# Kernel tuning notes

Measured on AMD Instinct MI355X. Metric: run time of the kernel, lower is better.

The kernel has to match this reference:

```python
import jax, jax.numpy as jnp
import numpy as np

D_MODEL = 1024
NUM_HEADS = 16
D_K = D_MODEL // NUM_HEADS


def setup_inputs() -> dict:
    key = jax.random.key(0)
    ks = jax.random.split(key, 11)
    B, S = 2, 2048
    scale = 1.0 / np.sqrt(D_MODEL)
    inp = {
        "q": jax.random.normal(ks[0], (B, S, D_MODEL), jnp.float32),
        "k": jax.random.normal(ks[1], (B, S, D_MODEL), jnp.float32),
        "v": jax.random.normal(ks[2], (B, S, D_MODEL), jnp.float32),
        "W_q": jax.random.normal(ks[3], (D_MODEL, D_MODEL), jnp.float32) * scale,
        "b_q": jnp.zeros((D_MODEL,), jnp.float32),
        "W_k": jax.random.normal(ks[4], (D_MODEL, D_MODEL), jnp.float32) * scale,
        "b_k": jnp.zeros((D_MODEL,), jnp.float32),
        "W_v": jax.random.normal(ks[5], (D_MODEL, D_MODEL), jnp.float32) * scale,
        "b_v": jnp.zeros((D_MODEL,), jnp.float32),
        "W_o": jax.random.normal(ks[6], (D_MODEL, D_MODEL), jnp.float32) * scale,
        "b_o": jnp.zeros((D_MODEL,), jnp.float32),
    }
    return inp


def _split_heads(x):
    B, S, _ = x.shape
    return x.reshape(B, S, NUM_HEADS, D_K).transpose(0, 2, 1, 3)  # [B,H,S,Dk]


def reference(q, k, v, W_q, b_q, W_k, b_k, W_v, b_v, W_o, b_o):
    # Linear projections (torch Linear: x @ W.T + b; here W stored as [in,out])
    qh = _split_heads(q @ W_q + b_q)  # [B,H,S,Dk]
    kh = _split_heads(k @ W_k + b_k)
    vh = _split_heads(v @ W_v + b_v)

    scores = jnp.einsum("bhqd,bhkd->bhqk", qh, kh) / jnp.sqrt(
        jnp.asarray(D_K, qh.dtype)
    )  # [B,H,S,S]
    probs = jax.nn.softmax(scores, axis=-1)
    ctx = jnp.einsum("bhqk,bhkd->bhqd", probs, vh)  # [B,H,S,Dk]

    B, H, S, Dk = ctx.shape
    out = ctx.transpose(0, 2, 1, 3).reshape(B, S, D_MODEL)
    return out @ W_o + b_o
```

## Files before the change

### kernel.cpp

```cpp
#include <hip/hip_runtime.h>
#include <stdint.h>

#define DM   1024
#define TOK  4096
#define SEQ  2048
#define NH   16
#define DKH  64
#define WELEM ((size_t)DM * DM)

typedef __bf16 bf16_t;
typedef bf16_t bf16x8 __attribute__((ext_vector_type(8)));
typedef _Float16 f16x8 __attribute__((ext_vector_type(8)));
typedef float  f32x16 __attribute__((ext_vector_type(16)));
typedef uint32_t u32x4 __attribute__((ext_vector_type(4)));

__device__ __forceinline__ uint16_t f2bf(float x) {
  uint32_t u = __builtin_bit_cast(uint32_t, x);
  u += 0x7fffu + ((u >> 16) & 1u);
  return (uint16_t)(u >> 16);
}
__device__ __forceinline__ uint16_t f2h(float x) {
  _Float16 h = (_Float16)x;
  return __builtin_bit_cast(uint16_t, h);
}
__device__ __forceinline__ uint32_t pkrtz(float a, float b) {
  auto h = __builtin_amdgcn_cvt_pkrtz(a, b);
  return __builtin_bit_cast(uint32_t, h);
}
__device__ __forceinline__ bf16x8 ldfrag(const uint16_t* p) {
  uint4 v = *(const uint4*)p;
  return __builtin_bit_cast(bf16x8, v);
}
__device__ __forceinline__ f16x8 ldfragh(const uint16_t* p) {
  uint4 v = *(const uint4*)p;
  return __builtin_bit_cast(f16x8, v);
}
__device__ __forceinline__ uint32_t cvtpk(float lo, float hi) {
  uint32_t r;
  asm("v_cvt_pk_bf16_f32 %0, %1, %2" : "=v"(r) : "v"(lo), "v"(hi));
  return r;
}
__device__ __forceinline__ void plswap(uint32_t& a, uint32_t& b) {
  asm("v_permlane32_swap_b32 %0, %1" : "+v"(a), "+v"(b));
}
__device__ __forceinline__ void gload_lds16(const void* g, void* l) {
  __builtin_amdgcn_global_load_lds(
      (const __attribute__((address_space(1))) uint32_t*)(g),
      (__attribute__((address_space(3))) uint32_t*)(l), 16, 0, 0);
}

__global__ void wsplit_kernel(const float* __restrict__ W0, const float* __restrict__ W1,
                              const float* __restrict__ W2, const float* __restrict__ W3,
                              uint16_t* __restrict__ hi) {
  const float* W = (blockIdx.z == 0) ? W0 : (blockIdx.z == 1) ? W1 : (blockIdx.z == 2) ? W2 : W3;
  uint16_t* hp = hi + blockIdx.z * WELEM;
  __shared__ float t[32][33];
  int n0 = blockIdx.x * 32, k0 = blockIdx.y * 32;
  int tx = threadIdx.x, ty = threadIdx.y;
#pragma unroll
  for (int i = 0; i < 4; i++) {
    int r = ty + i * 8;
    t[r][tx] = W[(size_t)(k0 + r) * DM + n0 + tx];
  }
  __syncthreads();
#pragma unroll
  for (int i = 0; i < 4; i++) {
    int r = ty + i * 8;
    hp[(size_t)(n0 + r) * DM + k0 + tx] = f2h(t[tx][r]);
  }
}

__global__ __launch_bounds__(256, 3) void proj_kernel(
    const float* __restrict__ A0, const float* __restrict__ A1, const float* __restrict__ A2,
    const uint16_t* __restrict__ Whi,
    const float* __restrict__ bA, const float* __restrict__ bB, const float* __restrict__ bC,
    uint16_t* __restrict__ oq, uint16_t* __restrict__ ok, uint16_t* __restrict__ ovt) {
  __shared__ __align__(16) char smem[49152];
  char* lA = smem;
  uint16_t* lBh = (uint16_t*)(smem + 32768);

  const int tid = threadIdx.x, lane = tid & 63, wid = tid >> 6;
  const int l31 = lane & 31, hi = lane >> 5;
  const int wr = wid >> 1, wc = wid & 1;
  const int bid = blockIdx.x, xcd = bid & 7, idx = bid >> 3;
  const int tm = xcd * 4 + (idx & 3), tn = idx >> 2;

  const int z = (int)blockIdx.y;
  const float* Ap = (z == 0) ? A0 : (z == 1) ? A1 : A2;
  const uint16_t* Bh = Whi + (size_t)z * WELEM;
  const float* bias = (z == 1) ? bB : (z == 2) ? bC : bA;

  f32x16 acc[2][2];
#pragma unroll
  for (int i = 0; i < 2; i++)
#pragma unroll
    for (int j = 0; j < 2; j++)
#pragma unroll
      for (int e = 0; e < 16; e++) acc[i][j][e] = 0.f;

  auto stage = [&](int buf, int kt) {
#pragma unroll
    for (int p = 0; p < 4; p++) {
      int sid = p * 256 + tid;
      int r = sid >> 3, cs = sid & 7;
      int g = cs ^ (r & 7);
      const float* src = Ap + (size_t)(tm * 128 + r) * DM + kt * 32 + g * 4;
      gload_lds16(src, lA + buf * 16384 + (p * 256 + wid * 64) * 16);
    }
#pragma unroll
    for (int p = 0; p < 2; p++) {
      int sid = p * 256 + tid;
      int r = sid >> 2, cs = sid & 3;
      int cg = cs ^ ((r >> 1) & 3);
      size_t offB = (size_t)(tn * 128 + r) * DM + kt * 32 + cg * 8;
      gload_lds16(Bh + offB, (char*)lBh + buf * 8192 + (p * 256 + wid * 64) * 16);
    }
  };

  stage(0, 0);
  for (int kt = 0; kt < DM / 32; kt++) {
    const int cur = kt & 1;
    __syncthreads();
    if (kt + 1 < DM / 32) stage(cur ^ 1, kt + 1);

    f16x8 af[2][2], bh[2][2];
#pragma unroll
    for (int ks = 0; ks < 2; ks++) {
      int cg4 = ks * 2 + hi;
#pragma unroll
      for (int rt = 0; rt < 2; rt++) {
        int rA = wr * 64 + rt * 32 + l31;
        const char* rowp = lA + cur * 16384 + rA * 128;
        uint4 u0 = *(const uint4*)(rowp + (((cg4 * 2)     ^ (rA & 7)) * 16));
        uint4 u1 = *(const uint4*)(rowp + (((cg4 * 2 + 1) ^ (rA & 7)) * 16));
        float4 f0 = __builtin_bit_cast(float4, u0);
        float4 f1 = __builtin_bit_cast(float4, u1);
        u32x4 uu;
        uu[0] = pkrtz(f0.x, f0.y); uu[1] = pkrtz(f0.z, f0.w);
        uu[2] = pkrtz(f1.x, f1.y); uu[3] = pkrtz(f1.z, f1.w);
        af[rt][ks] = __builtin_bit_cast(f16x8, uu);
      }
#pragma unroll
      for (int ct = 0; ct < 2; ct++) {
        int rB = wc * 64 + ct * 32 + l31;
        int cg = ks * 2 + hi;
        bh[ct][ks] = ldfragh(lBh + cur * 4096 + rB * 32 + (cg ^ ((rB >> 1) & 3)) * 8);
      }
    }
#pragma unroll
    for (int ks = 0; ks < 2; ks++)
#pragma unroll
      for (int rt = 0; rt < 2; rt++)
#pragma unroll
        for (int ct = 0; ct < 2; ct++)
          acc[rt][ct] = __builtin_amdgcn_mfma_f32_32x32x16_f16(af[rt][ks], bh[ct][ks], acc[rt][ct], 0, 0, 0);
  }

  if (z == 2) {
    __syncthreads();
    uint16_t* t16 = (uint16_t*)smem;
#pragma unroll
    for (int ct = 0; ct < 2; ct++) {
      int nl = wc * 64 + ct * 32 + l31;
      float bv = bias[tn * 128 + nl];
#pragma unroll
      for (int rt = 0; rt < 2; rt++)
#pragma unroll
        for (int g = 0; g < 16; g++) {
          int ml = wr * 64 + rt * 32 + (g & 3) + 8 * (g >> 2) + 4 * hi;
          t16[nl * 136 + ml] = f2bf(acc[rt][ct][g] + bv);
        }
    }
    __syncthreads();
    int nl2 = tid >> 1, mh = tid & 1;
    int ng = tn * 128 + nl2;
    int hh = ng >> 6, d = ng & 63;
    int b_ = tm >> 4, s0 = (tm & 15) * 128 + mh * 64;
    uint16_t* dst = ovt + (size_t)((b_ * NH + hh) * DKH + d) * SEQ + s0;
    const uint16_t* src = &t16[nl2 * 136 + mh * 64];
#pragma unroll
    for (int j = 0; j < 8; j++)
      ((uint4*)dst)[j] = ((const uint4*)src)[j];
  } else {
#pragma unroll
    for (int ct = 0; ct < 2; ct++) {
      int n = tn * 128 + wc * 64 + ct * 32 + l31;
      float bv = bias[n];
#pragma unroll
      for (int rt = 0; rt < 2; rt++)
#pragma unroll
        for (int g = 0; g < 16; g++) {
          int m = tm * 128 + wr * 64 + rt * 32 + (g & 3) + 8 * (g >> 2) + 4 * hi;
          float val = acc[rt][ct][g] + bv;
          if (z == 0) oq[(size_t)m * DM + n] = f2bf(val * 0.125f);
          else        ok[(size_t)m * DM + n] = f2bf(val);
        }
    }
  }
}

__global__ __launch_bounds__(256, 4) void proj_o_kernel(
    const uint16_t* __restrict__ A, const uint16_t* __restrict__ Bh,
    const float* __restrict__ bias, float* __restrict__ out) {
  __shared__ __attribute__((aligned(16))) uint16_t lA[2][128 * 32];
  __shared__ __attribute__((aligned(16))) uint16_t lBh[2][64 * 32];

  const int tid = threadIdx.x, lane = tid & 63, wid = tid >> 6;
  const int l31 = lane & 31, hi = lane >> 5;
  const int wr = wid >> 1, wc = wid & 1;
  const int bid = blockIdx.x, xcd = bid & 7, idx = bid >> 3;
  const int tm = xcd * 4 + (idx & 3), tn = idx >> 2;

  f32x16 acc[2];
#pragma unroll
  for (int i = 0; i < 2; i++)
#pragma unroll
    for (int e = 0; e < 16; e++) acc[i][e] = 0.f;

  auto stage = [&](int buf, int kt) {
#pragma unroll
    for (int p = 0; p < 2; p++) {
      int sid = p * 256 + tid;
      int r = sid >> 2, cs = sid & 3;
      int cg = cs ^ ((r >> 1) & 3);
      size_t offA = (size_t)(tm * 128 + r) * DM + kt * 32 + cg * 8;
      gload_lds16(A + offA, &lA[buf][(p * 256 + wid * 64) * 8]);
    }
    {
      int r = tid >> 2, cs = tid & 3;
      int cg = cs ^ ((r >> 1) & 3);
      size_t offB = (size_t)(tn * 64 + r) * DM + kt * 32 + cg * 8;
      gload_lds16(Bh + offB, &lBh[buf][wid * 64 * 8]);
    }
  };

  stage(0, 0);
  for (int kt = 0; kt < DM / 32; kt++) {
    const int cur = kt & 1;
    __syncthreads();
    if (kt + 1 < DM / 32) stage(cur ^ 1, kt + 1);

    f16x8 af[2][2], bh[2];
#pragma unroll
    for (int ks = 0; ks < 2; ks++) {
      int cg = ks * 2 + hi;
#pragma unroll
      for (int rt = 0; rt < 2; rt++) {
        int rA = wr * 64 + rt * 32 + l31;
        af[rt][ks] = ldfragh(&lA[cur][rA * 32 + (cg ^ ((rA >> 1) & 3)) * 8]);
      }
      int rB = wc * 32 + l31;
      bh[ks] = ldfragh(&lBh[cur][rB * 32 + (cg ^ ((rB >> 1) & 3)) * 8]);
    }
#pragma unroll
    for (int ks = 0; ks < 2; ks++)
#pragma unroll
      for (int rt = 0; rt < 2; rt++)
        acc[rt] = __builtin_amdgcn_mfma_f32_32x32x16_f16(af[rt][ks], bh[ks], acc[rt], 0, 0, 0);
  }

  const int n = tn * 64 + wc * 32 + l31;
  const float bv = bias[n];
#pragma unroll
  for (int rt = 0; rt < 2; rt++)
#pragma unroll
    for (int g = 0; g < 16; g++) {
      int m = tm * 128 + wr * 64 + rt * 32 + (g & 3) + 8 * (g >> 2) + 4 * hi;
      out[(size_t)m * DM + n] = acc[rt][g] + bv;
    }
}

__global__ __launch_bounds__(256, 2) void attn_kernel(
    const uint16_t* __restrict__ Qp, const uint16_t* __restrict__ Kp,
    const uint16_t* __restrict__ Vt, uint16_t* __restrict__ ctx) {
  __shared__ __align__(16) char smem[65536];
  uint16_t* lK = (uint16_t*)smem;
  uint16_t* lV = (uint16_t*)(smem + 32768);
  const int tid = threadIdx.x, lane = tid & 63, w = tid >> 6;
  const int q31 = lane & 31, hi = lane >> 5;
  const int bid = blockIdx.x, xcd = bid & 7, idx = bid >> 3;
  const int bh_ = xcd * 4 + (idx >> 4), qt = idx & 15;
  const int b = bh_ >> 4, h = bh_ & 15;
  const int bh = bh_;
  const float L2E = 1.44269504089f;
  const float MS = 20.0f * 1.44269504089f;

  auto stage = [&](int buf, int kt) {
#pragma unroll
    for (int p = 0; p < 4; p++) {
      int sid = p * 256 + tid;
      {
        int r = sid >> 3, cs = sid & 7;
        size_t gk = (size_t)(b * SEQ + kt * 128 + r) * DM + h * DKH + (cs ^ (r & 7)) * 8;
        gload_lds16(Kp + gk, lK + buf * 8192 + (p * 256 + w * 64) * 8);
      }
      {
        int r = sid >> 4, cs = sid & 15;
        size_t gv = (size_t)(bh * DKH + r) * SEQ + kt * 128 + (cs ^ (r & 7)) * 8;
        gload_lds16(Vt + gv, lV + buf * 8192 + (p * 256 + w * 64) * 8);
      }
    }
  };

  stage(0, 0);
  bf16x8 qf[4];
  const int qrow = b * SEQ + qt * 128 + w * 32 + q31;
#pragma unroll
  for (int d4 = 0; d4 < 4; d4++)
    qf[d4] = ldfrag(Qp + (size_t)qrow * DM + h * DKH + d4 * 16 + hi * 8);

  f32x16 zz;
#pragma unroll
  for (int i = 0; i < 16; i++) zz[i] = 0.f;
  f32x16 o0 = zz, o1 = zz;
  float l = 0.f;

  for (int kt = 0; kt < SEQ / 128; kt++) {
    const int cur = kt & 1;
    __syncthreads();
    if (kt + 1 < SEQ / 128) stage(cur ^ 1, kt + 1);

    __builtin_amdgcn_s_setprio(1);
    float s0 = 0.f, s1 = 0.f, s2 = 0.f, s3 = 0.f;
#pragma unroll
    for (int kb = 0; kb < 4; kb++) {
      f32x16 a = zz;
#pragma unroll
      for (int d4 = 0; d4 < 4; d4++) {
        int r = kb * 32 + q31;
        int slot = (d4 * 2 + hi) ^ (r & 7);
        bf16x8 kf = ldfrag(lK + cur * 8192 + r * 64 + slot * 8);
        a = __builtin_amdgcn_mfma_f32_32x32x16_bf16(kf, qf[d4], a, 0, 0, 0);
      }
#pragma unroll
      for (int r = 0; r < 16; r += 4) {
        float p0 = __builtin_amdgcn_exp2f(a[r + 0] * L2E - MS);
        float p1 = __builtin_amdgcn_exp2f(a[r + 1] * L2E - MS);
        float p2 = __builtin_amdgcn_exp2f(a[r + 2] * L2E - MS);
        float p3 = __builtin_amdgcn_exp2f(a[r + 3] * L2E - MS);
        a[r + 0] = p0; a[r + 1] = p1;
        a[r + 2] = p2; a[r + 3] = p3;
        s0 += p0; s1 += p1; s2 += p2; s3 += p3;
      }
      uint32_t wv[8];
#pragma unroll
      for (int i = 0; i < 8; i++) wv[i] = cvtpk(a[2 * i], a[2 * i + 1]);
      plswap(wv[0], wv[2]);
      plswap(wv[1], wv[3]);
      plswap(wv[4], wv[6]);
      plswap(wv[5], wv[7]);
      u32x4 c0, c1;
      c0[0] = wv[0]; c0[1] = wv[1]; c0[2] = wv[2]; c0[3] = wv[3];
      c1[0] = wv[4]; c1[1] = wv[5]; c1[2] = wv[6]; c1[3] = wv[7];
      bf16x8 p0f = __builtin_bit_cast(bf16x8, c0);
      bf16x8 p1f = __builtin_bit_cast(bf16x8, c1);
#pragma unroll
      for (int ks = 0; ks < 2; ks++) {
        bf16x8 pa = ks ? p1f : p0f;
        int cg = (kb * 2 + ks) * 2 + hi;
        {
          int r = q31;
          bf16x8 vf = ldfrag(lV + cur * 8192 + r * 128 + (cg ^ (r & 7)) * 8);
          o0 = __builtin_amdgcn_mfma_f32_32x32x16_bf16(vf, pa, o0, 0, 0, 0);
        }
        {
          int r = 32 + q31;
          bf16x8 vf = ldfrag(lV + cur * 8192 + r * 128 + (cg ^ (r & 7)) * 8);
          o1 = __builtin_amdgcn_mfma_f32_32x32x16_bf16(vf, pa, o1, 0, 0, 0);
        }
      }
    }
    __builtin_amdgcn_s_setprio(0);
    l += (s0 + s1) + (s2 + s3);
  }

  l += __shfl_xor(l, 32, 64);
  float rl = 1.f / l;
  __syncthreads();
  uint16_t* th = (uint16_t*)smem;
  int ql = w * 32 + q31;
#pragma unroll
  for (int g4 = 0; g4 < 4; g4++) {
    int d0 = g4 * 8 + hi * 4;
    ushort4 h0, h1;
#pragma unroll
    for (int e = 0; e < 4; e++) {
      ((uint16_t*)&h0)[e] = f2h(o0[g4 * 4 + e] * rl);
      ((uint16_t*)&h1)[e] = f2h(o1[g4 * 4 + e] * rl);
    }
    *(ushort4*)&th[ql * 72 + d0] = h0;
    *(ushort4*)&th[ql * 72 + 32 + d0] = h1;
  }
  __syncthreads();
  int qr = tid >> 1, dh = tid & 1;
  size_t obase = (size_t)(b * SEQ + qt * 128 + qr) * DM + h * DKH + dh * 32;
  const uint16_t* sh = &th[qr * 72 + dh * 32];
#pragma unroll
  for (int j = 0; j < 4; j++)
    ((uint4*)(ctx + obase))[j] = ((const uint4*)sh)[j];
}

extern "C" void kernel_launch(void* const* d_in, const int* in_sizes, int n_in,
                              void* d_out, int out_size, void* d_ws, size_t ws_size,
                              hipStream_t stream) {
  (void)in_sizes; (void)n_in; (void)out_size; (void)ws_size;
  const float* q  = (const float*)d_in[0];
  const float* k  = (const float*)d_in[1];
  const float* v  = (const float*)d_in[2];
  const float* Wq = (const float*)d_in[3];
  const float* bq = (const float*)d_in[4];
  const float* Wk = (const float*)d_in[5];
  const float* bk = (const float*)d_in[6];
  const float* Wv = (const float*)d_in[7];
  const float* bv = (const float*)d_in[8];
  const float* Wo = (const float*)d_in[9];
  const float* bo = (const float*)d_in[10];

  char* ws = (char*)d_ws;
  uint16_t* wt  = (uint16_t*)(ws + ((size_t)0 << 20));
  uint16_t* qp  = (uint16_t*)(ws + ((size_t)8 << 20));
  uint16_t* kp  = (uint16_t*)(ws + ((size_t)16 << 20));
  uint16_t* vt  = (uint16_t*)(ws + ((size_t)24 << 20));
  uint16_t* ctx = (uint16_t*)(ws + ((size_t)32 << 20));

  wsplit_kernel<<<dim3(32, 32, 4), dim3(32, 8), 0, stream>>>(Wq, Wk, Wv, Wo, wt);
  proj_kernel<<<dim3(256, 3), 256, 0, stream>>>(q, k, v, wt,
                                                bq, bk, bv, qp, kp, vt);
  attn_kernel<<<512, 256, 0, stream>>>(qp, kp, vt, ctx);
  proj_o_kernel<<<512, 256, 0, stream>>>(ctx, wt + 3 * WELEM, bo, (float*)d_out);
}
```

Measured before the change: 123.6 us.

## Convert A tile to fp16 in registers before LDS store in projection GEMM

The fp32 activation tile is no longer copied straight into LDS. It is now loaded into registers, converted to fp16 once per element, and stored to LDS in the same swizzled fp16 layout as the weights, with the store overlapping the MFMA work of the current stage. This halves the LDS footprint of the A buffer, so occupancy can rise from 3 to 4 blocks, and removes the repeated fp32-to-fp16 conversion on every fragment read. In exchange it adds register pressure for the prefetched float4s and issues synchronous global loads instead of direct-to-LDS loads.

```diff
diff --git a/kernel.cpp b/kernel.cpp
--- a/kernel.cpp
+++ b/kernel.cpp
@@ -70,14 +70,14 @@
   }
 }
 
-__global__ __launch_bounds__(256, 3) void proj_kernel(
+__global__ __launch_bounds__(256, 4) void proj_kernel(
     const float* __restrict__ A0, const float* __restrict__ A1, const float* __restrict__ A2,
     const uint16_t* __restrict__ Whi,
     const float* __restrict__ bA, const float* __restrict__ bB, const float* __restrict__ bC,
     uint16_t* __restrict__ oq, uint16_t* __restrict__ ok, uint16_t* __restrict__ ovt) {
-  __shared__ __align__(16) char smem[49152];
-  char* lA = smem;
-  uint16_t* lBh = (uint16_t*)(smem + 32768);
+  __shared__ __align__(16) char smem[36864];
+  uint16_t* lA  = (uint16_t*)smem;
+  uint16_t* lBh = (uint16_t*)(smem + 16384);
 
   const int tid = threadIdx.x, lane = tid & 63, wid = tid >> 6;
   const int l31 = lane & 31, hi = lane >> 5;
@@ -98,53 +98,68 @@
 #pragma unroll
       for (int e = 0; e < 16; e++) acc[i][j][e] = 0.f;
 
-  auto stage = [&](int buf, int kt) {
-#pragma unroll
-    for (int p = 0; p < 4; p++) {
+  float4 ar[2][2];
+
+  auto regloadA = [&](int kt) {
+#pragma unroll
+    for (int p = 0; p < 2; p++) {
       int sid = p * 256 + tid;
-      int r = sid >> 3, cs = sid & 7;
-      int g = cs ^ (r & 7);
-      const float* src = Ap + (size_t)(tm * 128 + r) * DM + kt * 32 + g * 4;
-      gload_lds16(src, lA + buf * 16384 + (p * 256 + wid * 64) * 16);
-    }
+      int r = sid >> 2, cs = sid & 3;
+      const float* src = Ap + (size_t)(tm * 128 + r) * DM + kt * 32 + cs * 8;
+      ar[p][0] = *(const float4*)(src);
+      ar[p][1] = *(const float4*)(src + 4);
+    }
+  };
+  auto writeA = [&](int buf) {
+#pragma unroll
+    for (int p = 0; p < 2; p++) {
+      int sid = p * 256 + tid;
+      int r = sid >> 2, cs = sid & 3;
+      int slot = cs ^ ((r >> 1) & 3);
+      u32x4 uu;
+      uu[0] = pkrtz(ar[p][0].x, ar[p][0].y);
+      uu[1] = pkrtz(ar[p][0].z, ar[p][0].w);
+      uu[2] = pkrtz(ar[p][1].x, ar[p][1].y);
+      uu[3] = pkrtz(ar[p][1].z, ar[p][1].w);
+      *(u32x4*)&lA[buf * 4096 + r * 32 + slot * 8] = uu;
+    }
+  };
+  auto stageB = [&](int buf, int kt) {
 #pragma unroll
     for (int p = 0; p < 2; p++) {
       int sid = p * 256 + tid;
       int r = sid >> 2, cs = sid & 3;
       int cg = cs ^ ((r >> 1) & 3);
       size_t offB = (size_t)(tn * 128 + r) * DM + kt * 32 + cg * 8;
-      gload_lds16(Bh + offB, (char*)lBh + buf * 8192 + (p * 256 + wid * 64) * 16);
+      gload_lds16(Bh + offB, &lBh[buf * 4096 + (p * 256 + wid * 64) * 8]);
     }
   };
 
-  stage(0, 0);
+  regloadA(0);
+  stageB(0, 0);
+  writeA(0);
+
   for (int kt = 0; kt < DM / 32; kt++) {
     const int cur = kt & 1;
     __syncthreads();
-    if (kt + 1 < DM / 32) stage(cur ^ 1, kt + 1);
+    if (kt + 1 < DM / 32) {
+      regloadA(kt + 1);
+      stageB(cur ^ 1, kt + 1);
+    }
 
     f16x8 af[2][2], bh[2][2];
 #pragma unroll
     for (int ks = 0; ks < 2; ks++) {
-      int cg4 = ks * 2 + hi;
+      int cg = ks * 2 + hi;
 #pragma unroll
       for (int rt = 0; rt < 2; rt++) {
         int rA = wr * 64 + rt * 32 + l31;
-        const char* rowp = lA + cur * 16384 + rA * 128;
-        uint4 u0 = *(const uint4*)(rowp + (((cg4 * 2)     ^ (rA & 7)) * 16));
-        uint4 u1 = *(const uint4*)(rowp + (((cg4 * 2 + 1) ^ (rA & 7)) * 16));
-        float4 f0 = __builtin_bit_cast(float4, u0);
-        float4 f1 = __builtin_bit_cast(float4, u1);
-        u32x4 uu;
-        uu[0] = pkrtz(f0.x, f0.y); uu[1] = pkrtz(f0.z, f0.w);
-        uu[2] = pkrtz(f1.x, f1.y); uu[3] = pkrtz(f1.z, f1.w);
-        af[rt][ks] = __builtin_bit_cast(f16x8, uu);
+        af[rt][ks] = ldfragh(&lA[cur * 4096 + rA * 32 + (cg ^ ((rA >> 1) & 3)) * 8]);
       }
 #pragma unroll
       for (int ct = 0; ct < 2; ct++) {
         int rB = wc * 64 + ct * 32 + l31;
-        int cg = ks * 2 + hi;
-        bh[ct][ks] = ldfragh(lBh + cur * 4096 + rB * 32 + (cg ^ ((rB >> 1) & 3)) * 8);
+        bh[ct][ks] = ldfragh(&lBh[cur * 4096 + rB * 32 + (cg ^ ((rB >> 1) & 3)) * 8]);
       }
     }
 #pragma unroll
@@ -154,6 +169,8 @@
 #pragma unroll
         for (int ct = 0; ct < 2; ct++)
           acc[rt][ct] = __builtin_amdgcn_mfma_f32_32x32x16_f16(af[rt][ks], bh[ct][ks], acc[rt][ct], 0, 0, 0);
+
+    if (kt + 1 < DM / 32) writeA(cur ^ 1);
   }
 
   if (z == 2) {
```

After: 122.9 us (median of 3 runs). Within noise of the previous version (-0.6%).
